# Kernel tuning notes

Measured on AMD Instinct MI355X. Metric: run time of the kernel, lower is better.

## Reference

```python
import jax, jax.numpy as jnp
import numpy as np

PATCH = 15  # box-filter kernel size (odd -> SAME padding == padding=PATCH//2, stride 1)


def _box_filter(x, k):
    """All-ones kxk conv2d, stride 1, zero pad k//2. x: (N,1,H,W).
    The ones kernel is separable: ones(k,k) = ones(k,1) @ ones(1,k)."""
    dn = ('NCHW', 'OIHW', 'NCHW')
    kh = jnp.ones((1, 1, k, 1), x.dtype)
    kw = jnp.ones((1, 1, 1, k), x.dtype)
    x = jax.lax.conv_general_dilated(x, kh, (1, 1), 'SAME', dimension_numbers=dn)
    x = jax.lax.conv_general_dilated(x, kw, (1, 1), 'SAME', dimension_numbers=dn)
    return x


def _rgb_to_yuv420(rgb):
    """rgb: (N,3,H,W) -> y:(N,H,W), u,v:(N,H/2,W/2) (2x2 avg-pooled chroma)."""
    r, g, b = rgb[:, 0], rgb[:, 1], rgb[:, 2]
    y = 0.299 * r + 0.587 * g + 0.114 * b
    u = -0.169 * r - 0.331 * g + 0.5 * b + 128.0
    v = 0.5 * r - 0.46 * g - 0.04 * b + 128.0
    n, h, w = u.shape
    u = u.reshape(n, h // 2, 2, w // 2, 2).mean(axis=(2, 4))
    v = v.reshape(n, h // 2, 2, w // 2, 2).mean(axis=(2, 4))
    return y, u, v


def _filtered_channels(img, k):
    y, u, v = _rgb_to_yuv420(img)
    return (_box_filter(y[:, None], k),
            _box_filter(u[:, None], k),
            _box_filter(v[:, None], k))


def setup_inputs() -> dict:
    key = jax.random.key(0)
    k1, k2 = jax.random.split(key)
    input_ = jax.random.uniform(k1, (16, 3, 512, 512), dtype=jnp.float32)
    target = jax.random.uniform(k2, (16, 3, 512, 512), dtype=jnp.float32)
    return {"input": input_, "target": target}


def reference(input, target):
    yi, ui, vi = _filtered_channels(input, PATCH)
    yt, ut, vt = _filtered_channels(target, PATCH)
    mse = lambda a, b: jnp.mean((a - b) ** 2)
    return mse(yi, yt) + mse(ui, ut) + mse(vi, vt)
```

## Files before the change

kernel.cpp:

```cpp
#include <hip/hip_runtime.h>

#define NIMG 16
#define H 512
#define W 512

static __device__ __forceinline__ void barln() {
    asm volatile("s_waitcnt lgkmcnt(0)" ::: "memory");
    __builtin_amdgcn_s_barrier();
    __builtin_amdgcn_sched_barrier(0);
}

#define ISSUE(p, A0,A1,A2,A3,A4,A5,A6,A7,A8,A9,A10,A11) do {                 \
    const int ya_ = 2*(p);                                                   \
    const int yb_ = ya_ + 1;                                                 \
    const int yca_ = ya_ < 0 ? 0 : (ya_ > H-1 ? H-1 : ya_);                  \
    const int ycb_ = yb_ < 0 ? 0 : (yb_ > H-1 ? H-1 : yb_);                  \
    const size_t oa_ = (size_t)yca_ * W + x;                                 \
    const size_t ob_ = (size_t)ycb_ * W + x;                                 \
    A0 = pi[oa_];  A1 = pi[plane+oa_];  A2 = pi[2*plane+oa_];                \
    A3 = pt[oa_];  A4 = pt[plane+oa_];  A5 = pt[2*plane+oa_];                \
    A6 = pi[ob_];  A7 = pi[plane+ob_];  A8 = pi[2*plane+ob_];                \
    A9 = pt[ob_];  A10= pt[plane+ob_];  A11= pt[2*plane+ob_];                \
} while (0)

__global__ __launch_bounds__(512, 2) void fused_row_kernel(
        const float* __restrict__ in, const float* __restrict__ tgt,
        float invY, float invC, float* __restrict__ partials) {
    __shared__ float ringY[16][512];
    __shared__ float ringC[16][512];
    __shared__ float LP[2][10][2][8];
    __shared__ float LS[2][10][2][8];
    __shared__ float CP[2][10][16];
    __shared__ float CS[2][10][16];
    __shared__ float part[8];

    const int tid = threadIdx.x;
    const int idx  = (blockIdx.x & 7) * 32 + (blockIdx.x >> 3);
    const int n    = idx >> 4;
    const int band = idx & 15;
    const int R0 = band << 5;
    const int P0 = band << 4;

    const size_t plane = (size_t)H * W;
    const float* pi = in  + (size_t)n * 3 * plane;
    const float* pt = tgt + (size_t)n * 3 * plane;

    const int x = tid;
    const int w = tid >> 6;
    const int l = tid & 63;

    const bool ev = (l & 1) == 0;
    const float kr = ev ? -0.169f : 0.5f;
    const float kg = ev ? -0.331f : -0.46f;
    const float kb = ev ? 0.5f    : -0.04f;

    for (int i = tid; i < 16 * 512; i += 512) {
        (&ringY[0][0])[i] = 0.f;
        (&ringC[0][0])[i] = 0.f;
    }
    if (tid < 320) {
        (&LP[0][0][0][0])[tid] = 0.f;
        (&LS[0][0][0][0])[tid] = 0.f;
        (&CP[0][0][0])[tid] = 0.f;
        (&CS[0][0][0])[tid] = 0.f;
    }
    __syncthreads();

    float svY = 0.f, svC = 0.f, accY = 0.f, accC = 0.f;

    auto STEP = [&](int p, int sp,
                    float v0, float v1, float v2, float v3, float v4, float v5,
                    float v6, float v7, float v8, float v9, float v10, float v11) {
        const float ma = ((unsigned)(2 * p)     < (unsigned)H) ? 1.f : 0.f;
        const float mb = ((unsigned)(2 * p + 1) < (unsigned)H) ? 1.f : 0.f;
        const float dra = (v0 - v3) * ma, dga = (v1 - v4)  * ma, dba = (v2 - v5)  * ma;
        const float drb = (v6 - v9) * mb, dgb = (v7 - v10) * mb, dbb = (v8 - v11) * mb;
        float Q0 = 0.299f * dra + 0.587f * dga + 0.114f * dba;
        float Q1 = 0.299f * drb + 0.587f * dgb + 0.114f * dbb;
        const float hr = dra + drb, hg = dga + dgb, hb2 = dba + dbb;
        const float sr = hr  + __shfl_xor(hr, 1, 64);
        const float sg = hg  + __shfl_xor(hg, 1, 64);
        const float sb = hb2 + __shfl_xor(hb2, 1, 64);
        float Qc = (kr * sr + kg * sg + kb * sb) * 0.25f;

#pragma unroll
        for (int d = 1; d <= 32; d <<= 1) {
            const float t0 = __shfl_up(Q0, d, 64);
            const float t1 = __shfl_up(Q1, d, 64);
            if (l >= d) { Q0 += t0; Q1 += t1; }
        }
#pragma unroll
        for (int d = 2; d <= 32; d <<= 1) {
            const float tc = __shfl_up(Qc, d, 64);
            if (l >= d) Qc += tc;
        }
        const float T0 = __shfl(Q0, 63, 64);
        const float T1 = __shfl(Q1, 63, 64);
        const float Tc = __shfl(Qc, 62 + (l & 1), 64);

        if (l < 7) {
            LP[sp][w + 1][0][l] = Q0;  LP[sp][w + 1][1][l] = Q1;
        } else if (l >= 56 && l < 63) {
            LS[sp][w + 1][0][l - 56] = T0 - Q0;
            LS[sp][w + 1][1][l - 56] = T1 - Q1;
        }
        if (l < 14)                  CP[sp][w + 1][l]      = Qc;
        else if (l >= 48 && l < 62)  CS[sp][w + 1][l - 48] = Tc - Qc;

        barln();

        const float d70 = __shfl_down(Q0, 7, 64);
        const float d71 = __shfl_down(Q1, 7, 64);
        const float u80 = __shfl_up(Q0, 8, 64);
        const float u81 = __shfl_up(Q1, 8, 64);
        float h0 = ((l <= 56) ? d70 : T0) - ((l >= 8) ? u80 : 0.f);
        float h1 = ((l <= 56) ? d71 : T1) - ((l >= 8) ? u81 : 0.f);
        if (l < 7)   { h0 += LS[sp][w][0][l];        h1 += LS[sp][w][1][l]; }
        if (l >= 57) { h0 += LP[sp][w + 2][0][l - 57]; h1 += LP[sp][w + 2][1][l - 57]; }
        const float dc = __shfl_down(Qc, 14, 64);
        const float uc = __shfl_up(Qc, 16, 64);
        float hc = ((l <= 49) ? dc : Tc) - ((l >= 16) ? uc : 0.f);
        if (l < 14)  hc += CS[sp][w][l];
        if (l >= 50) hc += CP[sp][w + 2][l - 50];

        const int ra = 2 * p, rb = ra + 1;
        svY += h0 - ringY[(ra + 1) & 15][x];
        { const int o = ra - 7; if ((unsigned)(o - R0) < 32u) accY += svY * svY; }
        svY += h1 - ringY[(ra + 2) & 15][x];
        { const int o = rb - 7; if ((unsigned)(o - R0) < 32u) accY += svY * svY; }
        ringY[ra & 15][x] = h0;
        ringY[rb & 15][x] = h1;
        svC += hc - ringC[(p + 1) & 15][x];
        { const int oc = p - 7; if ((unsigned)(oc - P0) < 16u) accC += svC * svC; }
        ringC[p & 15][x] = hc;
    };

    const int p0 = P0 - 7;
    float A0,A1,A2,A3,A4,A5,A6,A7,A8,A9,A10,A11;
    float B0,B1,B2,B3,B4,B5,B6,B7,B8,B9,B10,B11;
    ISSUE(p0, A0,A1,A2,A3,A4,A5,A6,A7,A8,A9,A10,A11);

#pragma unroll 1
    for (int it = 0; it < 15; ++it) {
        const int p = p0 + 2 * it;
        ISSUE(p + 1, B0,B1,B2,B3,B4,B5,B6,B7,B8,B9,B10,B11);
        STEP(p, 0, A0,A1,A2,A3,A4,A5,A6,A7,A8,A9,A10,A11);
        if (it < 14)
            ISSUE(p + 2, A0,A1,A2,A3,A4,A5,A6,A7,A8,A9,A10,A11);
        STEP(p + 1, 1, B0,B1,B2,B3,B4,B5,B6,B7,B8,B9,B10,B11);
    }

    float v = accY * invY + accC * invC;
    for (int o = 32; o > 0; o >>= 1) v += __shfl_down(v, o, 64);
    if (l == 0) part[w] = v;
    __syncthreads();
    if (tid == 0) {
        float s = 0.f;
#pragma unroll
        for (int j = 0; j < 8; ++j) s += part[j];
        partials[blockIdx.x] = s;
    }
}

__global__ void final_reduce_kernel(const float* __restrict__ partials, int n,
                                    float* __restrict__ out) {
    float s = 0.f;
    for (int i = threadIdx.x; i < n; i += 256) s += partials[i];
    for (int o = 32; o > 0; o >>= 1) s += __shfl_down(s, o, 64);
    __shared__ float part[4];
    const int lane = threadIdx.x & 63, wid = threadIdx.x >> 6;
    if (lane == 0) part[wid] = s;
    __syncthreads();
    if (threadIdx.x == 0)
        *out = part[0] + part[1] + part[2] + part[3];
}

extern "C" void kernel_launch(void* const* d_in, const int* in_sizes, int n_in,
                              void* d_out, int out_size, void* d_ws, size_t ws_size,
                              hipStream_t stream) {
    const float* input  = (const float*)d_in[0];
    const float* target = (const float*)d_in[1];
    float* out = (float*)d_out;
    float* partials = (float*)d_ws;

    const float invY = 1.0f / (float)((size_t)NIMG * H * W);
    const float invC = 1.0f / (float)((size_t)NIMG * (H/2) * (W/2));

    fused_row_kernel<<<256, 512, 0, stream>>>(input, target, invY, invC, partials);
    final_reduce_kernel<<<1, 256, 0, stream>>>(partials, 256, out);
}
```

Measured before the change: 142.0 us.

## Make each wave own an independent column strip with halo, dropping LDS and barriers

Replaces the 512-thread row-band kernel, which shared horizontal prefix halos through LDS with a barrier per step, with 256-thread blocks. In these, each wave processes a 32-column strip plus a 16-column halo on each side. The vertical box sums are kept in per-lane register rings, the horizontal sums use wave-local shuffles, and there is no LDS ring and no block-wide sync. Four times as many blocks are launched to raise parallelism. The cost is redundant loads and compute for the halo columns, since only half of each wave's lanes produce output.

```diff
diff --git a/kernel.cpp b/kernel.cpp
--- a/kernel.cpp
+++ b/kernel.cpp
@@ -4,162 +4,111 @@
 #define H 512
 #define W 512
 
-static __device__ __forceinline__ void barln() {
-    asm volatile("s_waitcnt lgkmcnt(0)" ::: "memory");
-    __builtin_amdgcn_s_barrier();
-    __builtin_amdgcn_sched_barrier(0);
-}
-
-#define ISSUE(p, A0,A1,A2,A3,A4,A5,A6,A7,A8,A9,A10,A11) do {                 \
-    const int ya_ = 2*(p);                                                   \
-    const int yb_ = ya_ + 1;                                                 \
-    const int yca_ = ya_ < 0 ? 0 : (ya_ > H-1 ? H-1 : ya_);                  \
-    const int ycb_ = yb_ < 0 ? 0 : (yb_ > H-1 ? H-1 : yb_);                  \
-    const size_t oa_ = (size_t)yca_ * W + x;                                 \
-    const size_t ob_ = (size_t)ycb_ * W + x;                                 \
-    A0 = pi[oa_];  A1 = pi[plane+oa_];  A2 = pi[2*plane+oa_];                \
-    A3 = pt[oa_];  A4 = pt[plane+oa_];  A5 = pt[2*plane+oa_];                \
-    A6 = pi[ob_];  A7 = pi[plane+ob_];  A8 = pi[2*plane+ob_];                \
-    A9 = pt[ob_];  A10= pt[plane+ob_];  A11= pt[2*plane+ob_];                \
-} while (0)
-
-__global__ __launch_bounds__(512, 2) void fused_row_kernel(
+__global__ __launch_bounds__(256, 4) void fused_wave_kernel(
         const float* __restrict__ in, const float* __restrict__ tgt,
         float invY, float invC, float* __restrict__ partials) {
-    __shared__ float ringY[16][512];
-    __shared__ float ringC[16][512];
-    __shared__ float LP[2][10][2][8];
-    __shared__ float LS[2][10][2][8];
-    __shared__ float CP[2][10][16];
-    __shared__ float CS[2][10][16];
-    __shared__ float part[8];
+    __shared__ float part[4];
 
     const int tid = threadIdx.x;
-    const int idx  = (blockIdx.x & 7) * 32 + (blockIdx.x >> 3);
-    const int n    = idx >> 4;
-    const int band = idx & 15;
-    const int R0 = band << 5;
-    const int P0 = band << 4;
+    const int wv  = tid >> 6;
+    const int l   = tid & 63;
+
+    const int g     = (blockIdx.x & 7) * 128 + (blockIdx.x >> 3);
+    const int n     = g >> 6;
+    const int band  = (g >> 2) & 15;
+    const int strip = ((g & 3) << 2) | wv;
 
     const size_t plane = (size_t)H * W;
     const float* pi = in  + (size_t)n * 3 * plane;
     const float* pt = tgt + (size_t)n * 3 * plane;
 
-    const int x = tid;
-    const int w = tid >> 6;
-    const int l = tid & 63;
+    const int x  = (strip << 5) - 16 + l;
+    const int xm = x < 0 ? 0 : (x > W - 1 ? W - 1 : x);
+    const float mx = (x == xm) ? 1.f : 0.f;
+    const float mL = (l >= 16 && l < 48) ? 1.f : 0.f;
 
     const bool ev = (l & 1) == 0;
     const float kr = ev ? -0.169f : 0.5f;
     const float kg = ev ? -0.331f : -0.46f;
     const float kb = ev ? 0.5f    : -0.04f;
 
-    for (int i = tid; i < 16 * 512; i += 512) {
-        (&ringY[0][0])[i] = 0.f;
-        (&ringC[0][0])[i] = 0.f;
-    }
-    if (tid < 320) {
-        (&LP[0][0][0][0])[tid] = 0.f;
-        (&LS[0][0][0][0])[tid] = 0.f;
-        (&CP[0][0][0])[tid] = 0.f;
-        (&CS[0][0][0])[tid] = 0.f;
-    }
-    __syncthreads();
+    const int yBase = (band << 5) - 14;
 
-    float svY = 0.f, svC = 0.f, accY = 0.f, accC = 0.f;
+    float ringA[8], ringB[8], ringC[16];
+#pragma unroll
+    for (int i = 0; i < 8; ++i) { ringA[i] = 0.f; ringB[i] = 0.f; }
+#pragma unroll
+    for (int i = 0; i < 16; ++i) ringC[i] = 0.f;
 
-    auto STEP = [&](int p, int sp,
-                    float v0, float v1, float v2, float v3, float v4, float v5,
-                    float v6, float v7, float v8, float v9, float v10, float v11) {
-        const float ma = ((unsigned)(2 * p)     < (unsigned)H) ? 1.f : 0.f;
-        const float mb = ((unsigned)(2 * p + 1) < (unsigned)H) ? 1.f : 0.f;
-        const float dra = (v0 - v3) * ma, dga = (v1 - v4)  * ma, dba = (v2 - v5)  * ma;
-        const float drb = (v6 - v9) * mb, dgb = (v7 - v10) * mb, dbb = (v8 - v11) * mb;
-        float Q0 = 0.299f * dra + 0.587f * dga + 0.114f * dba;
-        float Q1 = 0.299f * drb + 0.587f * dgb + 0.114f * dbb;
-        const float hr = dra + drb, hg = dga + dgb, hb2 = dba + dbb;
-        const float sr = hr  + __shfl_xor(hr, 1, 64);
-        const float sg = hg  + __shfl_xor(hg, 1, 64);
-        const float sb = hb2 + __shfl_xor(hb2, 1, 64);
-        float Qc = (kr * sr + kg * sg + kb * sb) * 0.25f;
+    float V = 0.f, Vc = 0.f, accY = 0.f, accC = 0.f;
 
-#pragma unroll
-        for (int d = 1; d <= 32; d <<= 1) {
-            const float t0 = __shfl_up(Q0, d, 64);
-            const float t1 = __shfl_up(Q1, d, 64);
-            if (l >= d) { Q0 += t0; Q1 += t1; }
-        }
-#pragma unroll
-        for (int d = 2; d <= 32; d <<= 1) {
-            const float tc = __shfl_up(Qc, d, 64);
-            if (l >= d) Qc += tc;
-        }
-        const float T0 = __shfl(Q0, 63, 64);
-        const float T1 = __shfl(Q1, 63, 64);
-        const float Tc = __shfl(Qc, 62 + (l & 1), 64);
+#define PAIR(q) do {                                                          \
+    const int yA = yBase + 2*(q), yB = yA + 1;                                \
+    const int yAc = yA < 0 ? 0 : (yA > H-1 ? H-1 : yA);                       \
+    const int yBc = yB < 0 ? 0 : (yB > H-1 ? H-1 : yB);                       \
+    const float mA = (yA == yAc) ? mx : 0.f;                                  \
+    const float mB = (yB == yBc) ? mx : 0.f;                                  \
+    const size_t oA = (size_t)yAc * W + xm;                                   \
+    const size_t oB = (size_t)yBc * W + xm;                                   \
+    const float irA = pi[oA], igA = pi[plane+oA], ibA = pi[2*plane+oA];       \
+    const float trA = pt[oA], tgA = pt[plane+oA], tbA = pt[2*plane+oA];       \
+    const float irB = pi[oB], igB = pi[plane+oB], ibB = pi[2*plane+oB];       \
+    const float trB = pt[oB], tgB = pt[plane+oB], tbB = pt[2*plane+oB];       \
+    const float drA = (irA-trA)*mA, dgA = (igA-tgA)*mA, dbA = (ibA-tbA)*mA;   \
+    const float drB = (irB-trB)*mB, dgB = (igB-tgB)*mB, dbB = (ibB-tbB)*mB;   \
+    const float dYA = 0.299f*drA + 0.587f*dgA + 0.114f*dbA;                   \
+    const float dYB = 0.299f*drB + 0.587f*dgB + 0.114f*dbB;                   \
+    const float Va = V + dYA - ringB[(q) & 7];           \
+    const float Vb = Va + dYB - ringA[((q)+1) & 7];      \
+    ringA[(q) & 7] = dYA;                                                     \
+    ringB[(q) & 7] = dYB;                                                     \
+    V = Vb;                                                                   \
+    if ((q) >= 10 && (q) <= 26) {             \
+        float PA = Va, PB = Vb;                                               \
+        _Pragma("unroll")                                                     \
+        for (int d = 1; d <= 32; d <<= 1) {                                   \
+            const float tA = __shfl_up(PA, d, 64);                            \
+            const float tB = __shfl_up(PB, d, 64);                            \
+            PA += (l >= d) ? tA : 0.f;                                        \
+            PB += (l >= d) ? tB : 0.f;                                        \
+        }                                                                     \
+        const float hA = __shfl_down(PA, 7, 64) - __shfl_up(PA, 8, 64);       \
+        const float hB = __shfl_down(PB, 7, 64) - __shfl_up(PB, 8, 64);       \
+        if ((q) >= 11) accY += hA * hA * mL;        \
+        if ((q) <= 25) accY += hB * hB * mL;        \
+    }                                                                         \
+    const float hr = drA + drB, hg = dgA + dgB, hb = dbA + dbB;               \
+    const float sr = hr + __shfl_xor(hr, 1, 64);                              \
+    const float sg = hg + __shfl_xor(hg, 1, 64);                              \
+    const float sb = hb + __shfl_xor(hb, 1, 64);                              \
+    const float Qc = (kr*sr + kg*sg + kb*sb) * 0.25f;                         \
+    Vc += Qc - ringC[((q)+1) & 15];                                           \
+    ringC[(q) & 15] = Qc;                                                     \
+    if ((q) >= 14 && (q) <= 29) {                \
+        float PC = Vc;                                                        \
+        _Pragma("unroll")                                                     \
+        for (int d = 2; d <= 32; d <<= 1) {                                   \
+            const float tC = __shfl_up(PC, d, 64);                            \
+            PC += (l >= d) ? tC : 0.f;                                        \
+        }                                                                     \
+        const float hc = __shfl_down(PC, 14, 64) - __shfl_up(PC, 16, 64);     \
+        accC += hc * hc * mL;                                                 \
+    }                                                                         \
+} while (0)
 
-        if (l < 7) {
-            LP[sp][w + 1][0][l] = Q0;  LP[sp][w + 1][1][l] = Q1;
-        } else if (l >= 56 && l < 63) {
-            LS[sp][w + 1][0][l - 56] = T0 - Q0;
-            LS[sp][w + 1][1][l - 56] = T1 - Q1;
-        }
-        if (l < 14)                  CP[sp][w + 1][l]      = Qc;
-        else if (l >= 48 && l < 62)  CS[sp][w + 1][l - 48] = Tc - Qc;
-
-        barln();
-
-        const float d70 = __shfl_down(Q0, 7, 64);
-        const float d71 = __shfl_down(Q1, 7, 64);
-        const float u80 = __shfl_up(Q0, 8, 64);
-        const float u81 = __shfl_up(Q1, 8, 64);
-        float h0 = ((l <= 56) ? d70 : T0) - ((l >= 8) ? u80 : 0.f);
-        float h1 = ((l <= 56) ? d71 : T1) - ((l >= 8) ? u81 : 0.f);
-        if (l < 7)   { h0 += LS[sp][w][0][l];        h1 += LS[sp][w][1][l]; }
-        if (l >= 57) { h0 += LP[sp][w + 2][0][l - 57]; h1 += LP[sp][w + 2][1][l - 57]; }
-        const float dc = __shfl_down(Qc, 14, 64);
-        const float uc = __shfl_up(Qc, 16, 64);
-        float hc = ((l <= 49) ? dc : Tc) - ((l >= 16) ? uc : 0.f);
-        if (l < 14)  hc += CS[sp][w][l];
-        if (l >= 50) hc += CP[sp][w + 2][l - 50];
-
-        const int ra = 2 * p, rb = ra + 1;
-        svY += h0 - ringY[(ra + 1) & 15][x];
-        { const int o = ra - 7; if ((unsigned)(o - R0) < 32u) accY += svY * svY; }
-        svY += h1 - ringY[(ra + 2) & 15][x];
-        { const int o = rb - 7; if ((unsigned)(o - R0) < 32u) accY += svY * svY; }
-        ringY[ra & 15][x] = h0;
-        ringY[rb & 15][x] = h1;
-        svC += hc - ringC[(p + 1) & 15][x];
-        { const int oc = p - 7; if ((unsigned)(oc - P0) < 16u) accC += svC * svC; }
-        ringC[p & 15][x] = hc;
-    };
-
-    const int p0 = P0 - 7;
-    float A0,A1,A2,A3,A4,A5,A6,A7,A8,A9,A10,A11;
-    float B0,B1,B2,B3,B4,B5,B6,B7,B8,B9,B10,B11;
-    ISSUE(p0, A0,A1,A2,A3,A4,A5,A6,A7,A8,A9,A10,A11);
-
-#pragma unroll 1
-    for (int it = 0; it < 15; ++it) {
-        const int p = p0 + 2 * it;
-        ISSUE(p + 1, B0,B1,B2,B3,B4,B5,B6,B7,B8,B9,B10,B11);
-        STEP(p, 0, A0,A1,A2,A3,A4,A5,A6,A7,A8,A9,A10,A11);
-        if (it < 14)
-            ISSUE(p + 2, A0,A1,A2,A3,A4,A5,A6,A7,A8,A9,A10,A11);
-        STEP(p + 1, 1, B0,B1,B2,B3,B4,B5,B6,B7,B8,B9,B10,B11);
-    }
+    PAIR(0);  PAIR(1);  PAIR(2);  PAIR(3);  PAIR(4);  PAIR(5);
+    PAIR(6);  PAIR(7);  PAIR(8);  PAIR(9);  PAIR(10); PAIR(11);
+    PAIR(12); PAIR(13); PAIR(14); PAIR(15); PAIR(16); PAIR(17);
+    PAIR(18); PAIR(19); PAIR(20); PAIR(21); PAIR(22); PAIR(23);
+    PAIR(24); PAIR(25); PAIR(26); PAIR(27); PAIR(28); PAIR(29);
+#undef PAIR
 
     float v = accY * invY + accC * invC;
     for (int o = 32; o > 0; o >>= 1) v += __shfl_down(v, o, 64);
-    if (l == 0) part[w] = v;
+    if (l == 0) part[wv] = v;
     __syncthreads();
-    if (tid == 0) {
-        float s = 0.f;
-#pragma unroll
-        for (int j = 0; j < 8; ++j) s += part[j];
-        partials[blockIdx.x] = s;
-    }
+    if (tid == 0)
+        partials[blockIdx.x] = (part[0] + part[1]) + (part[2] + part[3]);
 }
 
 __global__ void final_reduce_kernel(const float* __restrict__ partials, int n,
@@ -186,6 +135,6 @@
     const float invY = 1.0f / (float)((size_t)NIMG * H * W);
     const float invC = 1.0f / (float)((size_t)NIMG * (H/2) * (W/2));
 
-    fused_row_kernel<<<256, 512, 0, stream>>>(input, target, invY, invC, partials);
-    final_reduce_kernel<<<1, 256, 0, stream>>>(partials, 256, out);
+    fused_wave_kernel<<<1024, 256, 0, stream>>>(input, target, invY, invC, partials);
+    final_reduce_kernel<<<1, 256, 0, stream>>>(partials, 1024, out);
 }
```

Result: no change. 139.9 us (-1.4%).
